# Optimization experiments

Measured on AMD Instinct MI355X. Metric: run time of the kernel, lower is better.

## Reference

```python
import jax, jax.numpy as jnp
from jax import lax
import numpy as np

B, C, L = 32, 8, 512
C_IN = 512      # must equal L (tokenConv consumes permuted tensor)
D_MODEL = 512
SCALE_NUM = 64  # 63 actual scales


def build_wavelet_bank(scale_num, LB=-8.0, UB=8.0, N=1024, Fb=2.0, Fc=8.0):
    """Replicates cmor_torch; returns centered zero-padded kernel bank [S, K].
    Zero-centering is exact because every kernel length (16*s+1) is odd and K is odd,
    so the padded conv with pad=(K-1)//2 equals the original per-scale conv with
    pad=(k-1)//2."""
    x = np.linspace(LB, UB, N)
    wav = (np.pi * Fb) ** (-0.5) * np.exp(2j * np.pi * Fc * x) * np.exp(-x ** 2 / Fb)
    step = x[1] - x[0]
    kernels = []
    for scale in np.arange(1, scale_num):
        j = (np.arange(scale * (x[-1] - x[0]) + 1) / (scale * step)).astype(int)
        j = j[j < wav.size]
        kernels.append(np.real(wav[j]) * scale ** (-0.5))
    K = max(len(k) for k in kernels)
    if K % 2 == 0:
        K += 1
    bank = np.zeros((len(kernels), K), np.float32)
    for i, k in enumerate(kernels):
        assert (K - len(k)) % 2 == 0, "kernel parity mismatch"
        off = (K - len(k)) // 2
        bank[i, off:off + len(k)] = k
    return bank


def setup_inputs() -> dict:
    key = jax.random.key(0)
    k1, k2 = jax.random.split(key)
    x = jax.random.normal(k1, (B, C, L), dtype=jnp.float32)
    wavelet_bank = jnp.asarray(build_wavelet_bank(SCALE_NUM))  # [63, K]
    token_w = jax.random.normal(k2, (D_MODEL, C_IN, 3), dtype=jnp.float32) * 0.02
    return {"x": x, "wavelet_bank": wavelet_bank, "token_w": token_w}


def reference(x, wavelet_bank, token_w):
    Bb, Cc, Ll = x.shape
    S, K = wavelet_bank.shape
    pad = (K - 1) // 2
    # fused CWT over all (channel, scale) pairs: [B*C, 1, L] conv [S, 1, K] -> [B*C, S, L]
    xr = x.reshape(Bb * Cc, 1, Ll)
    conv = lax.conv_general_dilated(
        xr, wavelet_bank[:, None, :], window_strides=(1,),
        padding=[(pad, pad)], dimension_numbers=("NCH", "OIH", "NCH"))
    d = jnp.abs(jnp.diff(conv, axis=-1))                 # [B*C, S, L-1]
    d = jnp.concatenate([d, d[..., -1:]], axis=-1)       # replicate last sample -> L
    feats = d.reshape(Bb, Cc * S, Ll)
    out = jnp.concatenate([x, feats], axis=1)            # [B, C*(1+S), L]
    # tokenConv on permuted tensor: channels = L (= c_in), length = C*(1+S)
    h = out.transpose(0, 2, 1)                           # [B, L, C_total]
    hp = jnp.concatenate([h[..., -1:], h, h[..., :1]], axis=-1)  # circular pad=1
    y = lax.conv_general_dilated(
        hp, token_w, window_strides=(1,), padding="VALID",
        dimension_numbers=("NCH", "OIH", "NCH"))         # [B, d_model, C_total]
    return y.transpose(0, 2, 1)                          # [B, C_total, d_model]
```

## Files before the change

### kernel.cpp

```cpp
#include <hip/hip_runtime.h>
#include <hip/hip_bf16.h>

#define NB 32
#define NC 8
#define NL 512
#define NS 63
#define NK 1009
#define NPAD 504
#define ND 512
#define NCT 512
#define NROWS 514

typedef __attribute__((ext_vector_type(4))) float f32x4;
typedef __attribute__((ext_vector_type(8))) short short8;

#define APAD_BYTES (NB * NROWS * NL * 2)
#define WB_BYTES   (3 * ND * NL * 2)

typedef const __attribute__((address_space(1))) unsigned int* gp1_t;
typedef __attribute__((address_space(3))) unsigned int* lp3_t;
__device__ __forceinline__ void gload_lds16(const void* g, void* l) {
  __builtin_amdgcn_global_load_lds((gp1_t)g, (lp3_t)l, 16, 0, 0);
}

__device__ __forceinline__ unsigned short bf16_bits(float v) {
  return __builtin_bit_cast(unsigned short, __float2bfloat16(v));
}

#define WAITVM(N) asm volatile("s_waitcnt vmcnt(" #N ")" ::: "memory")
#define FENCE() asm volatile("" ::: "memory")
#define BAR() __builtin_amdgcn_s_barrier()
#define PRIO1() __builtin_amdgcn_s_setprio(1)
#define PRIO0() __builtin_amdgcn_s_setprio(0)

__global__ __launch_bounds__(256) void prep_kernel(
    const float* __restrict__ bank, const float* __restrict__ tw,
    __hip_bfloat16* __restrict__ Wb, __hip_bfloat16* __restrict__ bankB) {
  const int idx = blockIdx.x * 256 + threadIdx.x;

  {
    int i0 = idx * 4;
    const float4* t4 = (const float4*)(tw + (size_t)i0 * 3);
    float4 a = t4[0], bq = t4[1], c4 = t4[2];
    ushort4 w0 = make_ushort4(bf16_bits(a.x), bf16_bits(a.w), bf16_bits(bq.z), bf16_bits(c4.y));
    ushort4 w1 = make_ushort4(bf16_bits(a.y), bf16_bits(bq.x), bf16_bits(bq.w), bf16_bits(c4.z));
    ushort4 w2 = make_ushort4(bf16_bits(a.z), bf16_bits(bq.y), bf16_bits(c4.x), bf16_bits(c4.w));
    *(ushort4*)(Wb + 0 * ND * NL + i0) = w0;
    *(ushort4*)(Wb + 1 * ND * NL + i0) = w1;
    *(ushort4*)(Wb + 2 * ND * NL + i0) = w2;
  }
  {
    int s = idx >> 10, k = idx & 1023;
    float v = (s < NS && k < NK) ? bank[s * NK + k] : 0.f;
    bankB[idx] = __float2bfloat16(v);
  }
}

#define CPY8_STRIDE 3152

__global__ __launch_bounds__(512) void cwt_kernel(
    const float* __restrict__ x, const __hip_bfloat16* __restrict__ bankB,
    __hip_bfloat16* __restrict__ Apad) {
  __shared__ __align__(16) char smem[8 * 16384 + 8 * CPY8_STRIDE];
  char* bankS = smem;
  char* cpy = smem + 8 * 16384;

  const int tid = threadIdx.x;
  const int bc = blockIdx.x;
  const int b = bc >> 3, c = bc & 7;
  const int w = tid >> 6, l = tid & 63;
  const int hi = l >> 4, li = l & 15;
  const int r8 = l & 7;

  const float* xrow = x + bc * NL;

  if (tid < 512) {
    __hip_bfloat16 v = __float2bfloat16(xrow[tid]);
    Apad[((size_t)(b * NROWS) + 1 + c) * NL + tid] = v;
    if (c == 0) Apad[((size_t)(b * NROWS) + 513) * NL + tid] = v;
  }

  for (int i = 0; i < 13; ++i) {
    int p = tid + i * 512;
    if (p < 6176) {
      int r_ = p / 772;
      int pe = p - r_ * 772;
      int g0 = 2 * pe;
      int i0 = g0 - 8 + r_;
      float xa = (i0 >= NPAD && i0 < NPAD + NL) ? xrow[i0 - NPAD] : 0.f;
      float xb = (i0 + 1 >= NPAD && i0 + 1 < NPAD + NL) ? xrow[i0 + 1 - NPAD] : 0.f;
      float xc = (i0 + 2 >= NPAD && i0 + 2 < NPAD + NL) ? xrow[i0 + 2 - NPAD] : 0.f;
      unsigned u = (unsigned)bf16_bits(xb - xa) | ((unsigned)bf16_bits(xc - xb) << 16);
      *(unsigned*)(cpy + r_ * CPY8_STRIDE + g0 * 2) = u;
    }
  }

#define STAGE(kt)                                                             \
  {                                                                           \
    for (int i = 0; i < 2; ++i) {                                             \
      int ck = tid + i * 512;                                                 \
      int s_ = ck >> 4, rb = ck & 15;                                         \
      int srcc = rb ^ (s_ & 7);                                               \
      gload_lds16(bankB + s_ * 1024 + (kt) * 128 + srcc * 8,                  \
                  bankS + (kt) * 16384 + ck * 16);                            \
    }                                                                         \
  }

#define AVMM(kt, ksl, m)                                                       \
  {                                                                            \
    int srow = (m) * 16 + li;                                                  \
    int chunk = ((ksl) * 4 + hi) ^ (srow & 7);                                 \
    short8 av = *(const short8*)(bankS + (kt) * 16384 + srow * 256 + chunk * 16); \
    _Pragma("unroll") for (int n = 0; n < 4; ++n)                              \
      acc[m][n] = __builtin_amdgcn_mfma_f32_16x16x32_bf16(av, bv[n],           \
                                                          acc[m][n], 0, 0, 0); \
  }

#define CCOMP(kt, M0, M1, M2, M3)                                              \
  {                                                                            \
    _Pragma("unroll") for (int ksl = 0; ksl < 4; ++ksl) {                      \
      short8 bv[4];                                                            \
      _Pragma("unroll") for (int n = 0; n < 4; ++n) {                          \
        int ebyte = 16 + 2 * (tbase + n * 16 + 8 * (li >> 3) +                 \
                              (kt) * 128 + ksl * 32 + 8 * hi);                 \
        bv[n] = *(const short8*)(cpy + r8 * CPY8_STRIDE + ebyte);              \
      }                                                                        \
      if (M0) AVMM(kt, ksl, 0);                                                \
      if (M1) AVMM(kt, ksl, 1);                                                \
      if (M2) AVMM(kt, ksl, 2);                                                \
      if (M3) AVMM(kt, ksl, 3);                                                \
    }                                                                          \
  }

  STAGE(0); STAGE(1); STAGE(2); STAGE(3);
  STAGE(4); STAGE(5); STAGE(6); STAGE(7);

  f32x4 acc[4][4] = {};
  const int tbase = w * 64;

  asm volatile("s_waitcnt vmcnt(14) lgkmcnt(0)" ::: "memory");
  BAR(); FENCE(); CCOMP(0, 0, 0, 1, 1);
  WAITVM(12); BAR(); FENCE(); CCOMP(1, 0, 1, 1, 1);
  WAITVM(10); BAR(); FENCE(); CCOMP(2, 1, 1, 1, 1);
  WAITVM(8);  BAR(); FENCE(); CCOMP(3, 1, 1, 1, 1);
  WAITVM(6);  BAR(); FENCE(); CCOMP(4, 1, 1, 1, 1);
  WAITVM(4);  BAR(); FENCE(); CCOMP(5, 0, 1, 1, 1);
  WAITVM(2);  BAR(); FENCE(); CCOMP(6, 0, 0, 1, 1);
  WAITVM(0);  BAR(); FENCE(); CCOMP(7, 0, 0, 0, 1);

#pragma unroll
  for (int m = 0; m < 4; ++m) {
#pragma unroll
    for (int rg = 0; rg < 4; ++rg) {
      int s = m * 16 + hi * 4 + rg;
      if (s >= NS) continue;
      int ch = 8 + c * NS + s;
      size_t rowbase = ((size_t)(b * NROWS) + 1 + ch) * NL;
#pragma unroll
      for (int n = 0; n < 4; ++n) {
        int t = tbase + n * 16 + li;
        float d = fabsf(acc[m][n][rg]);
        __hip_bfloat16 hv = __float2bfloat16(d);
        bool lastgrp = (w == 7 && n == 3);
        bool skip = lastgrp && (li == 15);
        bool dup = lastgrp && (li == 14);
        if (!skip) Apad[rowbase + t] = hv;
        if (dup) Apad[rowbase + 511] = hv;
        if (ch == NCT - 1) {
          size_t wrapbase = (size_t)(b * NROWS) * NL;
          if (!skip) Apad[wrapbase + t] = hv;
          if (dup) Apad[wrapbase + 511] = hv;
        }
      }
    }
  }
#undef STAGE
#undef AVMM
#undef CCOMP
}

__global__ __launch_bounds__(512) void gemm_kernel(
    const __hip_bfloat16* __restrict__ Ap, const __hip_bfloat16* __restrict__ Wb,
    float* __restrict__ out) {
  __shared__ __hip_bfloat16 sA[3][256 * 64];
  __shared__ __hip_bfloat16 sB[3][128 * 64];

  const int tid = threadIdx.x;
  const int gid = blockIdx.x;
  const int idx = gid >> 3;
  const int mblk = (gid & 7) * 8 + (idx & 7);
  const int nblk = idx >> 3;
  const int b = mblk >> 1;
  const int p0 = (mblk & 1) * 256;
  const int o0 = nblk * 128;

  const int w = tid >> 6, lane = tid & 63;
  const int wm = w >> 1, wn = w & 1;
  const int row_in = lane & 15, hi = lane >> 4;

#define GSTAGE(kt, bu)                                                         \
  {                                                                            \
    const int kap_ = (kt) >> 3;                                                \
    const int l0_ = ((kt) & 7) << 6;                                           \
    _Pragma("unroll") for (int i = 0; i < 4; ++i) {                            \
      int ck = tid + i * 512;                                                  \
      int row = ck >> 3, cg = (ck & 7) ^ (row & 7);                            \
      gload_lds16(Ap + ((b * NROWS + p0 + kap_ + row) * NL + l0_ + cg * 8),    \
                  &sA[bu][ck * 8]);                                            \
    }                                                                          \
    _Pragma("unroll") for (int i = 0; i < 2; ++i) {                            \
      int ck = tid + i * 512;                                                  \
      int row = ck >> 3, cg = (ck & 7) ^ (row & 7);                            \
      gload_lds16(Wb + ((kap_ * ND + o0 + row) * NL + l0_ + cg * 8),           \
                  &sB[bu][ck * 8]);                                            \
    }                                                                          \
  }

#define KSLICE(bu, ks)                                                         \
  {                                                                            \
    short8 av[4], bv[4];                                                       \
    _Pragma("unroll") for (int m = 0; m < 4; ++m) {                            \
      int row = wm * 64 + m * 16 + row_in;                                     \
      int cs = ((ks) * 4 + hi) ^ (row & 7);                                    \
      av[m] = *(const short8*)(&sA[bu][(row * 8 + cs) * 8]);                   \
    }                                                                          \
    _Pragma("unroll") for (int n = 0; n < 4; ++n) {                            \
      int row = wn * 64 + n * 16 + row_in;                                     \
      int cs = ((ks) * 4 + hi) ^ (row & 7);                                    \
      bv[n] = *(const short8*)(&sB[bu][(row * 8 + cs) * 8]);                   \
    }                                                                          \
    PRIO1();                                                                   \
    _Pragma("unroll") for (int m = 0; m < 4; ++m)                              \
      _Pragma("unroll") for (int n = 0; n < 4; ++n)                            \
        acc[m][n] = __builtin_amdgcn_mfma_f32_16x16x32_bf16(av[m], bv[n],      \
                                                            acc[m][n], 0, 0, 0); \
    PRIO0();                                                                   \
  }

#define STEP(kt, bu, bs)                                                       \
  WAITVM(6); BAR(); FENCE();                                                   \
  GSTAGE((kt) + 2, bs);                                                        \
  KSLICE(bu, 0); KSLICE(bu, 1); FENCE();

  f32x4 acc[4][4] = {};

  GSTAGE(0, 0); GSTAGE(1, 1);

  for (int g = 0; g < 7; ++g) {
    const int kt = g * 3;
    STEP(kt + 0, 0, 2);
    STEP(kt + 1, 1, 0);
    STEP(kt + 2, 2, 1);
  }
  STEP(21, 0, 2);
  WAITVM(6); BAR(); FENCE(); KSLICE(1, 0); KSLICE(1, 1); FENCE();
  WAITVM(0); BAR(); FENCE(); KSLICE(2, 0); KSLICE(2, 1);
#undef GSTAGE
#undef KSLICE
#undef STEP

#pragma unroll
  for (int m = 0; m < 4; ++m) {
    const int p = p0 + wm * 64 + m * 16 + hi * 4;
#pragma unroll
    for (int n = 0; n < 4; ++n) {
      const int o = o0 + wn * 64 + n * 16 + row_in;
#pragma unroll
      for (int r = 0; r < 4; ++r)
        out[(size_t)((b * NCT) + p + r) * ND + o] = acc[m][n][r];
    }
  }
}

extern "C" void kernel_launch(void* const* d_in, const int* in_sizes, int n_in,
                              void* d_out, int out_size, void* d_ws, size_t ws_size,
                              hipStream_t stream) {
  const float* x = (const float*)d_in[0];
  const float* bank = (const float*)d_in[1];
  const float* tw = (const float*)d_in[2];
  float* out = (float*)d_out;

  char* ws = (char*)d_ws;
  __hip_bfloat16* Apad = (__hip_bfloat16*)ws;
  __hip_bfloat16* Wb = (__hip_bfloat16*)(ws + APAD_BYTES);
  __hip_bfloat16* bankB = (__hip_bfloat16*)(ws + APAD_BYTES + WB_BYTES);

  prep_kernel<<<256, 256, 0, stream>>>(bank, tw, Wb, bankB);
  cwt_kernel<<<256, 512, 0, stream>>>(x, bankB, Apad);
  gemm_kernel<<<256, 512, 0, stream>>>(Apad, Wb, out);
}
```

Measured before the change: 59.11 us.

## Pre-swizzle weights into MFMA fragment layout and load B directly to registers

The prep kernel now writes the bf16 token-conv weights in a fragment-ordered layout, so each lane can load its MFMA B operand straight from global memory with one 16-byte load. The GEMM drops the shared-memory B buffers and prefetches B fragments into three rotating register sets two K-steps ahead. A-tile global-to-LDS loads are split across the two k-slices to interleave with compute. This removes LDS traffic and LDS capacity for B, at the cost of more registers (24 extra short8 values) and more outstanding global loads, which changes the vmcnt wait thresholds.

```diff
diff --git a/kernel.cpp b/kernel.cpp
--- a/kernel.cpp
+++ b/kernel.cpp
@@ -15,7 +15,8 @@
 typedef __attribute__((ext_vector_type(8))) short short8;
 
 #define APAD_BYTES (NB * NROWS * NL * 2)
-#define WB_BYTES   (3 * ND * NL * 2)
+#define WBF_BYTES  (3 * ND * NL * 2)
+#define KAP_STRIDE (32 * 16 * 64 * 8)
 
 typedef const __attribute__((address_space(1))) unsigned int* gp1_t;
 typedef __attribute__((address_space(3))) unsigned int* lp3_t;
@@ -35,7 +36,7 @@
 
 __global__ __launch_bounds__(256) void prep_kernel(
     const float* __restrict__ bank, const float* __restrict__ tw,
-    __hip_bfloat16* __restrict__ Wb, __hip_bfloat16* __restrict__ bankB) {
+    __hip_bfloat16* __restrict__ WbF, __hip_bfloat16* __restrict__ bankB) {
   const int idx = blockIdx.x * 256 + threadIdx.x;
 
   {
@@ -45,9 +46,13 @@
     ushort4 w0 = make_ushort4(bf16_bits(a.x), bf16_bits(a.w), bf16_bits(bq.z), bf16_bits(c4.y));
     ushort4 w1 = make_ushort4(bf16_bits(a.y), bf16_bits(bq.x), bf16_bits(bq.w), bf16_bits(c4.z));
     ushort4 w2 = make_ushort4(bf16_bits(a.z), bf16_bits(bq.y), bf16_bits(c4.x), bf16_bits(c4.w));
-    *(ushort4*)(Wb + 0 * ND * NL + i0) = w0;
-    *(ushort4*)(Wb + 1 * ND * NL + i0) = w1;
-    *(ushort4*)(Wb + 2 * ND * NL + i0) = w2;
+    int o = i0 >> 9, l = i0 & 511;
+    int og = o >> 4, ri = o & 15;
+    int ksg = l >> 5, h2 = (l >> 3) & 3, e0 = l & 7;
+    int base = ((og * 16 + ksg) * 64 + (ri + 16 * h2)) * 8 + e0;
+    *(ushort4*)(WbF + 0 * KAP_STRIDE + base) = w0;
+    *(ushort4*)(WbF + 1 * KAP_STRIDE + base) = w1;
+    *(ushort4*)(WbF + 2 * KAP_STRIDE + base) = w2;
   }
   {
     int s = idx >> 10, k = idx & 1023;
@@ -180,10 +185,9 @@
 }
 
 __global__ __launch_bounds__(512) void gemm_kernel(
-    const __hip_bfloat16* __restrict__ Ap, const __hip_bfloat16* __restrict__ Wb,
+    const __hip_bfloat16* __restrict__ Ap, const __hip_bfloat16* __restrict__ WbF,
     float* __restrict__ out) {
   __shared__ __hip_bfloat16 sA[3][256 * 64];
-  __shared__ __hip_bfloat16 sB[3][128 * 64];
 
   const int tid = threadIdx.x;
   const int gid = blockIdx.x;
@@ -197,66 +201,75 @@
   const int w = tid >> 6, lane = tid & 63;
   const int wm = w >> 1, wn = w & 1;
   const int row_in = lane & 15, hi = lane >> 4;
-
-#define GSTAGE(kt, bu)                                                         \
+  const int og0 = (o0 >> 4) + wn * 4;
+
+#define GS_A(kt, bu, i0, i1)                                                   \
   {                                                                            \
     const int kap_ = (kt) >> 3;                                                \
     const int l0_ = ((kt) & 7) << 6;                                           \
-    _Pragma("unroll") for (int i = 0; i < 4; ++i) {                            \
+    _Pragma("unroll") for (int i = (i0); i <= (i1); ++i) {                     \
       int ck = tid + i * 512;                                                  \
       int row = ck >> 3, cg = (ck & 7) ^ (row & 7);                            \
       gload_lds16(Ap + ((b * NROWS + p0 + kap_ + row) * NL + l0_ + cg * 8),    \
                   &sA[bu][ck * 8]);                                            \
     }                                                                          \
-    _Pragma("unroll") for (int i = 0; i < 2; ++i) {                            \
-      int ck = tid + i * 512;                                                  \
-      int row = ck >> 3, cg = (ck & 7) ^ (row & 7);                            \
-      gload_lds16(Wb + ((kap_ * ND + o0 + row) * NL + l0_ + cg * 8),           \
-                  &sB[bu][ck * 8]);                                            \
-    }                                                                          \
-  }
-
-#define KSLICE(bu, ks)                                                         \
-  {                                                                            \
-    short8 av[4], bv[4];                                                       \
+  }
+
+#define BVL(ktn, SET, ks)                                                      \
+  {                                                                            \
+    const int kap_ = (ktn) >> 3;                                               \
+    const int ksg_ = ((ktn) & 7) * 2 + (ks);                                   \
+    _Pragma("unroll") for (int n = 0; n < 4; ++n)                              \
+      SET[(ks) * 4 + n] = *(const short8*)(                                    \
+          WbF + (((kap_ * 32 + og0 + n) * 16 + ksg_) * 64 + lane) * 8);        \
+  }
+
+#define SLICE(bu, ks, CUR, STG)                                                \
+  {                                                                            \
+    short8 av[4];                                                              \
     _Pragma("unroll") for (int m = 0; m < 4; ++m) {                            \
       int row = wm * 64 + m * 16 + row_in;                                     \
       int cs = ((ks) * 4 + hi) ^ (row & 7);                                    \
       av[m] = *(const short8*)(&sA[bu][(row * 8 + cs) * 8]);                   \
     }                                                                          \
-    _Pragma("unroll") for (int n = 0; n < 4; ++n) {                            \
-      int row = wn * 64 + n * 16 + row_in;                                     \
-      int cs = ((ks) * 4 + hi) ^ (row & 7);                                    \
-      bv[n] = *(const short8*)(&sB[bu][(row * 8 + cs) * 8]);                   \
-    }                                                                          \
+    STG;                                                                       \
     PRIO1();                                                                   \
     _Pragma("unroll") for (int m = 0; m < 4; ++m)                              \
       _Pragma("unroll") for (int n = 0; n < 4; ++n)                            \
-        acc[m][n] = __builtin_amdgcn_mfma_f32_16x16x32_bf16(av[m], bv[n],      \
-                                                            acc[m][n], 0, 0, 0); \
+        acc[m][n] = __builtin_amdgcn_mfma_f32_16x16x32_bf16(                   \
+            av[m], CUR[(ks) * 4 + n], acc[m][n], 0, 0, 0);                     \
     PRIO0();                                                                   \
   }
 
-#define STEP(kt, bu, bs)                                                       \
-  WAITVM(6); BAR(); FENCE();                                                   \
-  GSTAGE((kt) + 2, bs);                                                        \
-  KSLICE(bu, 0); KSLICE(bu, 1); FENCE();
+#define STEP(kt, bu, bs, CUR, NXT)                                             \
+  WAITVM(20); BAR(); FENCE();                                                  \
+  SLICE(bu, 0, CUR, { GS_A((kt) + 2, bs, 0, 1); BVL((kt) + 2, NXT, 0); });     \
+  SLICE(bu, 1, CUR, { GS_A((kt) + 2, bs, 2, 3); BVL((kt) + 2, NXT, 1); });     \
+  FENCE();
 
   f32x4 acc[4][4] = {};
-
-  GSTAGE(0, 0); GSTAGE(1, 1);
+  short8 bvA[8], bvB[8], bvC[8];
+
+  GS_A(0, 0, 0, 3);
+  GS_A(1, 1, 0, 3);
+  BVL(0, bvA, 0); BVL(0, bvA, 1);
+  BVL(1, bvB, 0); BVL(1, bvB, 1);
+  FENCE();
 
   for (int g = 0; g < 7; ++g) {
     const int kt = g * 3;
-    STEP(kt + 0, 0, 2);
-    STEP(kt + 1, 1, 0);
-    STEP(kt + 2, 2, 1);
-  }
-  STEP(21, 0, 2);
-  WAITVM(6); BAR(); FENCE(); KSLICE(1, 0); KSLICE(1, 1); FENCE();
-  WAITVM(0); BAR(); FENCE(); KSLICE(2, 0); KSLICE(2, 1);
-#undef GSTAGE
-#undef KSLICE
+    STEP(kt + 0, 0, 2, bvA, bvC);
+    STEP(kt + 1, 1, 0, bvB, bvA);
+    STEP(kt + 2, 2, 1, bvC, bvB);
+  }
+  STEP(21, 0, 2, bvA, bvC);
+  WAITVM(20); BAR(); FENCE();
+  SLICE(1, 0, bvB, (void)0); SLICE(1, 1, bvB, (void)0); FENCE();
+  WAITVM(8); BAR(); FENCE();
+  SLICE(2, 0, bvC, (void)0); SLICE(2, 1, bvC, (void)0);
+#undef GS_A
+#undef BVL
+#undef SLICE
 #undef STEP
 
 #pragma unroll
@@ -282,10 +295,10 @@
 
   char* ws = (char*)d_ws;
   __hip_bfloat16* Apad = (__hip_bfloat16*)ws;
-  __hip_bfloat16* Wb = (__hip_bfloat16*)(ws + APAD_BYTES);
-  __hip_bfloat16* bankB = (__hip_bfloat16*)(ws + APAD_BYTES + WB_BYTES);
-
-  prep_kernel<<<256, 256, 0, stream>>>(bank, tw, Wb, bankB);
+  __hip_bfloat16* WbF = (__hip_bfloat16*)(ws + APAD_BYTES);
+  __hip_bfloat16* bankB = (__hip_bfloat16*)(ws + APAD_BYTES + WBF_BYTES);
+
+  prep_kernel<<<256, 256, 0, stream>>>(bank, tw, WbF, bankB);
   cwt_kernel<<<256, 512, 0, stream>>>(x, bankB, Apad);
-  gemm_kernel<<<256, 512, 0, stream>>>(Apad, Wb, out);
-}
+  gemm_kernel<<<256, 512, 0, stream>>>(Apad, WbF, out);
+}
```

Measured after the change: 59.04 us. Within noise of the previous version (-0.1%).
